# Kernel tuning notes

Hardware: AMD Instinct MI355X
Metric: run time of the kernel (lower is better)

The kernel has to match this reference:

```python
import jax, jax.numpy as jnp
import numpy as np

N = 100000
E = 1600000
IN_DIM, HID, OUT_DIM = 128, 128, 64


def setup_inputs() -> dict:
    key = jax.random.key(0)
    ks = jax.random.split(key, 8)
    x = jax.random.normal(ks[0], (N, IN_DIM), dtype=jnp.float32)
    edge_index = jax.random.randint(ks[1], (2, E), 0, N, dtype=jnp.int64)
    def glorot(k, fan_in, fan_out):
        lim = np.sqrt(6.0 / (fan_in + fan_out)).astype(np.float32)
        return jax.random.uniform(k, (fan_in, fan_out), jnp.float32, -lim, lim)
    W1 = glorot(ks[2], IN_DIM, HID)
    b1 = jnp.zeros((HID,), jnp.float32)
    W2 = glorot(ks[3], HID, HID)
    b2 = jnp.zeros((HID,), jnp.float32)
    W3 = glorot(ks[4], HID, OUT_DIM)
    b3 = jnp.zeros((OUT_DIM,), jnp.float32)
    return {"x": x, "edge_index": edge_index, "W1": W1, "b1": b1,
            "W2": W2, "b2": b2, "W3": W3, "b3": b3}


def _gcn_norm(edge_index, num_nodes):
    # PyG gcn_norm with add_self_loops=True, edge_weight=1:
    # A_hat = A + I, deg over destination (col), norm = d^-1/2[src]*d^-1/2[dst]
    loop = jnp.arange(num_nodes, dtype=edge_index.dtype)
    src = jnp.concatenate([edge_index[0], loop])
    dst = jnp.concatenate([edge_index[1], loop])
    deg = jax.ops.segment_sum(jnp.ones_like(dst, dtype=jnp.float32), dst,
                              num_segments=num_nodes)
    dinv = jnp.where(deg > 0, jax.lax.rsqrt(deg), 0.0)
    norm = dinv[src] * dinv[dst]  # [E + N]
    return src, dst, norm


def _gcn_conv(x, W, b, src, dst, norm, num_nodes):
    h = x @ W                                   # [N, out] linear transform
    msg = h[src] * norm[:, None]                # gather + normalize
    out = jax.ops.segment_sum(msg, dst, num_segments=num_nodes)  # scatter-add
    return out + b


def reference(x, edge_index, W1, b1, W2, b2, W3, b3):
    num_nodes = x.shape[0]
    src, dst, norm = _gcn_norm(edge_index, num_nodes)
    h = jax.nn.relu(_gcn_conv(x, W1, b1, src, dst, norm, num_nodes))
    h = jax.nn.relu(_gcn_conv(h, W2, b2, src, dst, norm, num_nodes))
    out = _gcn_conv(h, W3, b3, src, dst, norm, num_nodes)
    return out
```

## Files before the change

### kernel.cpp

```cpp
#include <hip/hip_runtime.h>
#include <hip/hip_bf16.h>

typedef __attribute__((ext_vector_type(8))) short bf16x8;
typedef __attribute__((ext_vector_type(4))) float f32x4;

#define NPB 32
#define BCAP 768
#define NSHARD 8
#define SCAP 160
#define CURSTRIDE 16


static __device__ __forceinline__ unsigned short f2bf(float f) {
    unsigned int u = __float_as_uint(f);
    unsigned int r = (u + 0x7fffu + ((u >> 16) & 1u)) >> 16;
    return (unsigned short)r;
}
static __device__ __forceinline__ float bflo(unsigned int v) {
    return __uint_as_float(v << 16);
}
static __device__ __forceinline__ float bfhi(unsigned int v) {
    return __uint_as_float(v & 0xffff0000u);
}


__global__ void k_bin(const int* __restrict__ src, const int* __restrict__ dst, int E,
                      int NB, int* __restrict__ scur, unsigned* __restrict__ recs) {
    int e = blockIdx.x * blockDim.x + threadIdx.x;
    const int shard = blockIdx.x & (NSHARD - 1);
    if (e < E) {
        int s = src[e], d = dst[e];
        int b = d >> 5;
        int pos = atomicAdd(&scur[(shard * NB + b) * CURSTRIDE], 1);
        if (pos < SCAP)
            recs[((size_t)shard * NB + b) * SCAP + pos] = ((unsigned)s << 5) | (unsigned)(d & 31);
    }
}

__global__ __launch_bounds__(256) void k_build(const unsigned* __restrict__ recs,
                                               const int* __restrict__ scur, int n, int NB,
                                               float* __restrict__ dinv,
                                               int* __restrict__ rp, int* __restrict__ re,
                                               int* __restrict__ col) {
    __shared__ unsigned lrec[BCAP];
    __shared__ int c32[NPB], x32[NPB], cur32[NPB];
    const int b = blockIdx.x;
    const int t = threadIdx.x;
    const size_t base = (size_t)b * BCAP;

    int cp[NSHARD + 1];
    cp[0] = 0;
#pragma unroll
    for (int s = 0; s < NSHARD; ++s) {
        int c = scur[(s * NB + b) * CURSTRIDE];
        c = (c < SCAP) ? c : SCAP;
        cp[s + 1] = cp[s] + c;
    }
    const int cnt = (cp[NSHARD] < BCAP) ? cp[NSHARD] : BCAP;

#pragma unroll
    for (int s = 0; s < NSHARD; ++s) {
        const unsigned* seg = recs + ((size_t)s * NB + b) * SCAP;
        const int c = cp[s + 1] - cp[s];
        for (int k = t; k < c; k += 256) {
            int o = cp[s] + k;
            if (o < BCAP) lrec[o] = seg[k];
        }
    }
    if (t < NPB) c32[t] = 0;
    __syncthreads();
    for (int k = t; k < cnt; k += 256) atomicAdd(&c32[lrec[k] & (NPB - 1)], 1);
    __syncthreads();
    if (t == 0) {
        int run = 0;
        for (int j = 0; j < NPB; ++j) { x32[j] = run; run += c32[j]; }
    }
    __syncthreads();
    if (t < NPB) {
        int node = b * NPB + t;
        if (node < n) {
            dinv[node] = rsqrtf((float)c32[t] + 1.0f);
            rp[node] = (int)base + x32[t];
            re[node] = (int)base + x32[t] + c32[t];
        }
        cur32[t] = x32[t];
    }
    __syncthreads();
    for (int k = t; k < cnt; k += 256) {
        unsigned r = lrec[k];
        int node = r & (NPB - 1);
        int slot = atomicAdd(&cur32[node], 1);
        col[base + slot] = (int)(r >> 5);
    }
}


__global__ void k_wsplit(const float* __restrict__ W, int C,
                         unsigned short* __restrict__ Wt_hi,
                         unsigned short* __restrict__ Wt_lo) {
    int idx = blockIdx.x * 256 + threadIdx.x;
    if (idx >= C * 128) return;
    int c = idx >> 7;
    int k = idx & 127;
    float a = W[k * C + c];
    unsigned short h = f2bf(a);
    float hf = __uint_as_float((unsigned int)h << 16);
    Wt_hi[idx] = h;
    Wt_lo[idx] = f2bf(a - hf);
}


template <int OUTD, bool BF16OUT>
__global__ __launch_bounds__(512, 4) void k_gemm_mfma(
    const float* __restrict__ A, const unsigned short* __restrict__ Wt_hi,
    const unsigned short* __restrict__ Wt_lo, void* __restrict__ houtp,
    int ntiles) {
    __shared__ unsigned short Ah[32 * 128];
    __shared__ unsigned short Al[32 * 128];
    const int t = threadIdx.x;
    const int wave = t >> 6, lane = t & 63;
    const int l15 = lane & 15, l4 = lane >> 4;

    const int cb = (OUTD == 128) ? wave : (wave & 3);
    const int s0 = (OUTD == 128) ? 0 : (wave >> 2);

    bf16x8 wh[4], wl[4];
    {
        const int c = cb * 16 + l15;
#pragma unroll
        for (int kk = 0; kk < 4; ++kk) {
            const int off = c * 128 + kk * 32 + l4 * 8;
            wh[kk] = *(const bf16x8*)&Wt_hi[off];
            wl[kk] = *(const bf16x8*)&Wt_lo[off];
        }
    }

    const int srow = t >> 4;
    const int sk0 = (t & 15) * 8;
    const int sboff = (srow * 256 + sk0 * 2) ^ ((srow & 7) << 4);

    for (int mt = blockIdx.x; mt < ntiles; mt += gridDim.x) {
        __syncthreads();
        {
            const float* src = A + ((size_t)mt * 32 + srow) * 128 + sk0;
            float4 a0 = *(const float4*)src;
            float4 a1 = *(const float4*)(src + 4);
            float av[8] = {a0.x, a0.y, a0.z, a0.w, a1.x, a1.y, a1.z, a1.w};
            bf16x8 hv, lv;
#pragma unroll
            for (int j = 0; j < 8; ++j) {
                unsigned short h = f2bf(av[j]);
                float hf = __uint_as_float((unsigned int)h << 16);
                hv[j] = (short)h;
                lv[j] = (short)f2bf(av[j] - hf);
            }
            *(bf16x8*)((char*)Ah + sboff) = hv;
            *(bf16x8*)((char*)Al + sboff) = lv;
        }
        __syncthreads();

        f32x4 acc0 = {0.f, 0.f, 0.f, 0.f};
        f32x4 acc1 = {0.f, 0.f, 0.f, 0.f};
        const int row0 = s0 * 16 + l15;
        const int xo = (l15 & 7) << 4;
#pragma unroll
        for (int kk = 0; kk < 4; ++kk) {
            const int off = kk * 64 + l4 * 16;
            bf16x8 a0h = *(const bf16x8*)((const char*)Ah + ((row0 * 256 + off) ^ xo));
            bf16x8 a0l = *(const bf16x8*)((const char*)Al + ((row0 * 256 + off) ^ xo));
            if (OUTD == 128) {
                bf16x8 a1h = *(const bf16x8*)((const char*)Ah + (((16 + l15) * 256 + off) ^ xo));
                bf16x8 a1l = *(const bf16x8*)((const char*)Al + (((16 + l15) * 256 + off) ^ xo));
                acc0 = __builtin_amdgcn_mfma_f32_16x16x32_bf16(a0h, wh[kk], acc0, 0, 0, 0);
                acc1 = __builtin_amdgcn_mfma_f32_16x16x32_bf16(a1h, wh[kk], acc1, 0, 0, 0);
                acc0 = __builtin_amdgcn_mfma_f32_16x16x32_bf16(a0l, wh[kk], acc0, 0, 0, 0);
                acc1 = __builtin_amdgcn_mfma_f32_16x16x32_bf16(a1l, wh[kk], acc1, 0, 0, 0);
                acc0 = __builtin_amdgcn_mfma_f32_16x16x32_bf16(a0h, wl[kk], acc0, 0, 0, 0);
                acc1 = __builtin_amdgcn_mfma_f32_16x16x32_bf16(a1h, wl[kk], acc1, 0, 0, 0);
            } else {
                acc0 = __builtin_amdgcn_mfma_f32_16x16x32_bf16(a0h, wh[kk], acc0, 0, 0, 0);
                acc0 = __builtin_amdgcn_mfma_f32_16x16x32_bf16(a0l, wh[kk], acc0, 0, 0, 0);
                acc0 = __builtin_amdgcn_mfma_f32_16x16x32_bf16(a0h, wl[kk], acc0, 0, 0, 0);
            }
        }

        const size_t rbase = (size_t)mt * 32;
        const int c = cb * 16 + l15;
#pragma unroll
        for (int q = 0; q < 4; ++q) {
            size_t r0 = rbase + (size_t)(s0 * 16 + l4 * 4 + q);
            if (BF16OUT) {
                ((unsigned short*)houtp)[r0 * OUTD + c] = f2bf(acc0[q]);
            } else {
                ((float*)houtp)[r0 * OUTD + c] = acc0[q];
            }
            if (OUTD == 128) {
                size_t r1 = rbase + (size_t)(16 + l4 * 4 + q);
                if (BF16OUT) {
                    ((unsigned short*)houtp)[r1 * OUTD + c] = f2bf(acc1[q]);
                } else {
                    ((float*)houtp)[r1 * OUTD + c] = acc1[q];
                }
            }
        }
    }
}


template <bool RELU>
__global__ void k_agg128_bf16(const unsigned int* __restrict__ hb,
                              const int* __restrict__ rp, const int* __restrict__ re,
                              const int* __restrict__ col, const float* __restrict__ dinv,
                              const float* __restrict__ b, float2* __restrict__ out, int n) {
    const int i = blockIdx.x;
    const int t = threadIdx.x;
    const float di = dinv[i];
    unsigned int self = hb[(size_t)i * 64 + t];
    float2 bb = ((const float2*)b)[t];
    float acc0 = bb.x + di * di * bflo(self);
    float acc1 = bb.y + di * di * bfhi(self);
    int e = rp[i];
    const int e1 = re[i];
    for (; e + 4 <= e1; e += 4) {
        int s0 = col[e], s1 = col[e + 1], s2 = col[e + 2], s3 = col[e + 3];
        float w0 = dinv[s0] * di, w1 = dinv[s1] * di;
        float w2 = dinv[s2] * di, w3 = dinv[s3] * di;
        unsigned int v0 = hb[(size_t)s0 * 64 + t];
        unsigned int v1 = hb[(size_t)s1 * 64 + t];
        unsigned int v2 = hb[(size_t)s2 * 64 + t];
        unsigned int v3 = hb[(size_t)s3 * 64 + t];
        acc0 += w0 * bflo(v0); acc1 += w0 * bfhi(v0);
        acc0 += w1 * bflo(v1); acc1 += w1 * bfhi(v1);
        acc0 += w2 * bflo(v2); acc1 += w2 * bfhi(v2);
        acc0 += w3 * bflo(v3); acc1 += w3 * bfhi(v3);
    }
    for (; e < e1; ++e) {
        int s = col[e];
        float w = dinv[s] * di;
        unsigned int v = hb[(size_t)s * 64 + t];
        acc0 += w * bflo(v); acc1 += w * bfhi(v);
    }
    if (RELU) { acc0 = fmaxf(acc0, 0.0f); acc1 = fmaxf(acc1, 0.0f); }
    out[(size_t)i * 64 + t] = make_float2(acc0, acc1);
}


__global__ void k_agg64_f32(const float* __restrict__ h, const int* __restrict__ rp,
                            const int* __restrict__ re, const int* __restrict__ col,
                            const float* __restrict__ dinv, const float* __restrict__ b,
                            float* __restrict__ out, int n) {
    const int i = blockIdx.x;
    const int d = threadIdx.x;
    const float di = dinv[i];
    float acc = b[d] + di * di * h[(size_t)i * 64 + d];
    int e = rp[i];
    const int e1 = re[i];
    for (; e + 4 <= e1; e += 4) {
        int s0 = col[e], s1 = col[e + 1], s2 = col[e + 2], s3 = col[e + 3];
        float w0 = dinv[s0] * di, w1 = dinv[s1] * di;
        float w2 = dinv[s2] * di, w3 = dinv[s3] * di;
        acc += w0 * h[(size_t)s0 * 64 + d];
        acc += w1 * h[(size_t)s1 * 64 + d];
        acc += w2 * h[(size_t)s2 * 64 + d];
        acc += w3 * h[(size_t)s3 * 64 + d];
    }
    for (; e < e1; ++e) {
        int s = col[e];
        acc += dinv[s] * di * h[(size_t)s * 64 + d];
    }
    out[(size_t)i * 64 + d] = acc;
}


extern "C" void kernel_launch(void* const* d_in, const int* in_sizes, int n_in,
                              void* d_out, int out_size, void* d_ws, size_t ws_size,
                              hipStream_t stream) {
    const float* x  = (const float*)d_in[0];
    const int*   ei = (const int*)d_in[1];
    const float* W1 = (const float*)d_in[2];
    const float* b1 = (const float*)d_in[3];
    const float* W2 = (const float*)d_in[4];
    const float* b2 = (const float*)d_in[5];
    const float* W3 = (const float*)d_in[6];
    const float* b3 = (const float*)d_in[7];
    float* out = (float*)d_out;

    const int n = in_sizes[0] / 128;
    const int E = in_sizes[1] / 2;
    const int* srcA = ei;
    const int* dstA = ei + E;
    const int NB = (n + NPB - 1) / NPB;

    char* ws = (char*)d_ws;
    size_t off = 0;
    auto alloc = [&](size_t bytes) -> void* {
        off = (off + 255) & ~(size_t)255;
        void* p = ws + off;
        off += bytes;
        return p;
    };

    void*  h    = alloc((size_t)n * 128 * 2);
    float* agg  = (float*)alloc((size_t)n * 128 * 4);
    unsigned* recs = (unsigned*)agg;
    float* dinv = (float*)alloc((size_t)n * 4);
    int*   rp   = (int*)alloc((size_t)n * 4);
    int*   re   = (int*)alloc((size_t)n * 4);
    int*   scur = (int*)alloc((size_t)NSHARD * NB * CURSTRIDE * 4);
    int*   col  = (int*)alloc((size_t)NB * BCAP * 4);
    unsigned short* W1h = (unsigned short*)alloc(128 * 128 * 2);
    unsigned short* W1l = (unsigned short*)alloc(128 * 128 * 2);
    unsigned short* W2h = (unsigned short*)alloc(128 * 128 * 2);
    unsigned short* W2l = (unsigned short*)alloc(128 * 128 * 2);
    unsigned short* W3h = (unsigned short*)alloc(64 * 128 * 2);
    unsigned short* W3l = (unsigned short*)alloc(64 * 128 * 2);

    hipMemsetAsync(scur, 0, (size_t)NSHARD * NB * CURSTRIDE * 4, stream);
    k_bin<<<(E + 255) / 256, 256, 0, stream>>>(srcA, dstA, E, NB, scur, recs);
    k_build<<<NB, 256, 0, stream>>>(recs, scur, n, NB, dinv, rp, re, col);

    k_wsplit<<<(128 * 128 + 255) / 256, 256, 0, stream>>>(W1, 128, W1h, W1l);
    k_wsplit<<<(128 * 128 + 255) / 256, 256, 0, stream>>>(W2, 128, W2h, W2l);
    k_wsplit<<<(64 * 128 + 255) / 256, 256, 0, stream>>>(W3, 64, W3h, W3l);

    const int ntiles = n / 32;
    const int gblocks = 1024;

    k_gemm_mfma<128, true><<<gblocks, 512, 0, stream>>>(x, W1h, W1l, h, ntiles);
    k_agg128_bf16<true><<<n, 64, 0, stream>>>((const unsigned int*)h, rp, re, col, dinv, b1,
                                              (float2*)agg, n);
    k_gemm_mfma<128, true><<<gblocks, 512, 0, stream>>>(agg, W2h, W2l, h, ntiles);
    k_agg128_bf16<true><<<n, 64, 0, stream>>>((const unsigned int*)h, rp, re, col, dinv, b2,
                                              (float2*)agg, n);
    k_gemm_mfma<64, false><<<gblocks, 512, 0, stream>>>(agg, W3h, W3l, h, ntiles);
    k_agg64_f32<<<n, 64, 0, stream>>>((const float*)h, rp, re, col, dinv, b3, out, n);
}
```

Measured before the change: 443.9 us.

## Store intermediate activations in bf16 and gather bf16 features in final aggregation

Aggregation outputs are now written as packed bf16 instead of fp32. The next GEMM loads them directly into shared memory and drops the low-part split and its MFMA pass. The last GEMM now emits bf16, and a new 64-wide aggregation kernel packs 8 nodes per 256-thread block and gathers bf16 pairs. The three weight-split launches are merged into one. This halves gather and intermediate traffic and removes some MFMA work, at the cost of extra rounding error on intermediate activations.

```diff
diff --git a/kernel.cpp b/kernel.cpp
--- a/kernel.cpp
+++ b/kernel.cpp
@@ -95,28 +95,36 @@
 }
 
 
-__global__ void k_wsplit(const float* __restrict__ W, int C,
-                         unsigned short* __restrict__ Wt_hi,
-                         unsigned short* __restrict__ Wt_lo) {
+__global__ void k_wsplit_all(const float* __restrict__ W1, const float* __restrict__ W2,
+                             const float* __restrict__ W3,
+                             unsigned short* __restrict__ W1h, unsigned short* __restrict__ W1l,
+                             unsigned short* __restrict__ W2h, unsigned short* __restrict__ W2l,
+                             unsigned short* __restrict__ W3h, unsigned short* __restrict__ W3l) {
     int idx = blockIdx.x * 256 + threadIdx.x;
-    if (idx >= C * 128) return;
+    const float* W;
+    unsigned short *Wh, *Wl;
+    int C;
+    if (idx < 16384) { W = W1; Wh = W1h; Wl = W1l; C = 128; }
+    else if (idx < 32768) { idx -= 16384; W = W2; Wh = W2h; Wl = W2l; C = 128; }
+    else if (idx < 40960) { idx -= 32768; W = W3; Wh = W3h; Wl = W3l; C = 64; }
+    else return;
     int c = idx >> 7;
     int k = idx & 127;
     float a = W[k * C + c];
     unsigned short h = f2bf(a);
     float hf = __uint_as_float((unsigned int)h << 16);
-    Wt_hi[idx] = h;
-    Wt_lo[idx] = f2bf(a - hf);
-}
-
-
-template <int OUTD, bool BF16OUT>
+    Wh[idx] = h;
+    Wl[idx] = f2bf(a - hf);
+}
+
+
+template <int OUTD, bool AF32, bool BF16OUT>
 __global__ __launch_bounds__(512, 4) void k_gemm_mfma(
-    const float* __restrict__ A, const unsigned short* __restrict__ Wt_hi,
+    const void* __restrict__ Ap, const unsigned short* __restrict__ Wt_hi,
     const unsigned short* __restrict__ Wt_lo, void* __restrict__ houtp,
     int ntiles) {
     __shared__ unsigned short Ah[32 * 128];
-    __shared__ unsigned short Al[32 * 128];
+    __shared__ unsigned short Al[AF32 ? 32 * 128 : 64];
     const int t = threadIdx.x;
     const int wave = t >> 6, lane = t & 63;
     const int l15 = lane & 15, l4 = lane >> 4;
@@ -141,8 +149,8 @@
 
     for (int mt = blockIdx.x; mt < ntiles; mt += gridDim.x) {
         __syncthreads();
-        {
-            const float* src = A + ((size_t)mt * 32 + srow) * 128 + sk0;
+        if (AF32) {
+            const float* src = (const float*)Ap + ((size_t)mt * 32 + srow) * 128 + sk0;
             float4 a0 = *(const float4*)src;
             float4 a1 = *(const float4*)(src + 4);
             float av[8] = {a0.x, a0.y, a0.z, a0.w, a1.x, a1.y, a1.z, a1.w};
@@ -156,6 +164,10 @@
             }
             *(bf16x8*)((char*)Ah + sboff) = hv;
             *(bf16x8*)((char*)Al + sboff) = lv;
+        } else {
+            const unsigned short* src =
+                (const unsigned short*)Ap + ((size_t)mt * 32 + srow) * 128 + sk0;
+            *(bf16x8*)((char*)Ah + sboff) = *(const bf16x8*)src;
         }
         __syncthreads();
 
@@ -167,20 +179,25 @@
         for (int kk = 0; kk < 4; ++kk) {
             const int off = kk * 64 + l4 * 16;
             bf16x8 a0h = *(const bf16x8*)((const char*)Ah + ((row0 * 256 + off) ^ xo));
-            bf16x8 a0l = *(const bf16x8*)((const char*)Al + ((row0 * 256 + off) ^ xo));
             if (OUTD == 128) {
                 bf16x8 a1h = *(const bf16x8*)((const char*)Ah + (((16 + l15) * 256 + off) ^ xo));
-                bf16x8 a1l = *(const bf16x8*)((const char*)Al + (((16 + l15) * 256 + off) ^ xo));
                 acc0 = __builtin_amdgcn_mfma_f32_16x16x32_bf16(a0h, wh[kk], acc0, 0, 0, 0);
                 acc1 = __builtin_amdgcn_mfma_f32_16x16x32_bf16(a1h, wh[kk], acc1, 0, 0, 0);
-                acc0 = __builtin_amdgcn_mfma_f32_16x16x32_bf16(a0l, wh[kk], acc0, 0, 0, 0);
-                acc1 = __builtin_amdgcn_mfma_f32_16x16x32_bf16(a1l, wh[kk], acc1, 0, 0, 0);
                 acc0 = __builtin_amdgcn_mfma_f32_16x16x32_bf16(a0h, wl[kk], acc0, 0, 0, 0);
                 acc1 = __builtin_amdgcn_mfma_f32_16x16x32_bf16(a1h, wl[kk], acc1, 0, 0, 0);
+                if (AF32) {
+                    bf16x8 a0l = *(const bf16x8*)((const char*)Al + ((row0 * 256 + off) ^ xo));
+                    bf16x8 a1l = *(const bf16x8*)((const char*)Al + (((16 + l15) * 256 + off) ^ xo));
+                    acc0 = __builtin_amdgcn_mfma_f32_16x16x32_bf16(a0l, wh[kk], acc0, 0, 0, 0);
+                    acc1 = __builtin_amdgcn_mfma_f32_16x16x32_bf16(a1l, wh[kk], acc1, 0, 0, 0);
+                }
             } else {
                 acc0 = __builtin_amdgcn_mfma_f32_16x16x32_bf16(a0h, wh[kk], acc0, 0, 0, 0);
-                acc0 = __builtin_amdgcn_mfma_f32_16x16x32_bf16(a0l, wh[kk], acc0, 0, 0, 0);
                 acc0 = __builtin_amdgcn_mfma_f32_16x16x32_bf16(a0h, wl[kk], acc0, 0, 0, 0);
+                if (AF32) {
+                    bf16x8 a0l = *(const bf16x8*)((const char*)Al + ((row0 * 256 + off) ^ xo));
+                    acc0 = __builtin_amdgcn_mfma_f32_16x16x32_bf16(a0l, wh[kk], acc0, 0, 0, 0);
+                }
             }
         }
 
@@ -211,7 +228,8 @@
 __global__ void k_agg128_bf16(const unsigned int* __restrict__ hb,
                               const int* __restrict__ rp, const int* __restrict__ re,
                               const int* __restrict__ col, const float* __restrict__ dinv,
-                              const float* __restrict__ b, float2* __restrict__ out, int n) {
+                              const float* __restrict__ b, unsigned int* __restrict__ outb,
+                              int n) {
     const int i = blockIdx.x;
     const int t = threadIdx.x;
     const float di = dinv[i];
@@ -241,34 +259,45 @@
         acc0 += w * bflo(v); acc1 += w * bfhi(v);
     }
     if (RELU) { acc0 = fmaxf(acc0, 0.0f); acc1 = fmaxf(acc1, 0.0f); }
-    out[(size_t)i * 64 + t] = make_float2(acc0, acc1);
-}
-
-
-__global__ void k_agg64_f32(const float* __restrict__ h, const int* __restrict__ rp,
-                            const int* __restrict__ re, const int* __restrict__ col,
-                            const float* __restrict__ dinv, const float* __restrict__ b,
-                            float* __restrict__ out, int n) {
-    const int i = blockIdx.x;
-    const int d = threadIdx.x;
+    outb[(size_t)i * 64 + t] = (unsigned)f2bf(acc0) | ((unsigned)f2bf(acc1) << 16);
+}
+
+
+__global__ void k_agg64_bf16(const unsigned int* __restrict__ hb,
+                             const int* __restrict__ rp, const int* __restrict__ re,
+                             const int* __restrict__ col, const float* __restrict__ dinv,
+                             const float* __restrict__ b, float2* __restrict__ out, int n) {
+    const int t = threadIdx.x;
+    const int i = blockIdx.x * 8 + (t >> 5);
+    const int ln = t & 31;
+    if (i >= n) return;
     const float di = dinv[i];
-    float acc = b[d] + di * di * h[(size_t)i * 64 + d];
+    unsigned int self = hb[(size_t)i * 32 + ln];
+    float2 bb = ((const float2*)b)[ln];
+    float acc0 = bb.x + di * di * bflo(self);
+    float acc1 = bb.y + di * di * bfhi(self);
     int e = rp[i];
     const int e1 = re[i];
     for (; e + 4 <= e1; e += 4) {
         int s0 = col[e], s1 = col[e + 1], s2 = col[e + 2], s3 = col[e + 3];
         float w0 = dinv[s0] * di, w1 = dinv[s1] * di;
         float w2 = dinv[s2] * di, w3 = dinv[s3] * di;
-        acc += w0 * h[(size_t)s0 * 64 + d];
-        acc += w1 * h[(size_t)s1 * 64 + d];
-        acc += w2 * h[(size_t)s2 * 64 + d];
-        acc += w3 * h[(size_t)s3 * 64 + d];
+        unsigned int v0 = hb[(size_t)s0 * 32 + ln];
+        unsigned int v1 = hb[(size_t)s1 * 32 + ln];
+        unsigned int v2 = hb[(size_t)s2 * 32 + ln];
+        unsigned int v3 = hb[(size_t)s3 * 32 + ln];
+        acc0 += w0 * bflo(v0); acc1 += w0 * bfhi(v0);
+        acc0 += w1 * bflo(v1); acc1 += w1 * bfhi(v1);
+        acc0 += w2 * bflo(v2); acc1 += w2 * bfhi(v2);
+        acc0 += w3 * bflo(v3); acc1 += w3 * bfhi(v3);
     }
     for (; e < e1; ++e) {
         int s = col[e];
-        acc += dinv[s] * di * h[(size_t)s * 64 + d];
-    }
-    out[(size_t)i * 64 + d] = acc;
+        float w = dinv[s] * di;
+        unsigned int v = hb[(size_t)s * 32 + ln];
+        acc0 += w * bflo(v); acc1 += w * bfhi(v);
+    }
+    out[(size_t)i * 32 + ln] = make_float2(acc0, acc1);
 }
 
 
@@ -301,7 +330,7 @@
     };
 
     void*  h    = alloc((size_t)n * 128 * 2);
-    float* agg  = (float*)alloc((size_t)n * 128 * 4);
+    void*  agg  = alloc((size_t)n * 128 * 2);
     unsigned* recs = (unsigned*)agg;
     float* dinv = (float*)alloc((size_t)n * 4);
     int*   rp   = (int*)alloc((size_t)n * 4);
@@ -319,19 +348,18 @@
     k_bin<<<(E + 255) / 256, 256, 0, stream>>>(srcA, dstA, E, NB, scur, recs);
     k_build<<<NB, 256, 0, stream>>>(recs, scur, n, NB, dinv, rp, re, col);
 
-    k_wsplit<<<(128 * 128 + 255) / 256, 256, 0, stream>>>(W1, 128, W1h, W1l);
-    k_wsplit<<<(128 * 128 + 255) / 256, 256, 0, stream>>>(W2, 128, W2h, W2l);
-    k_wsplit<<<(64 * 128 + 255) / 256, 256, 0, stream>>>(W3, 64, W3h, W3l);
+    k_wsplit_all<<<160, 256, 0, stream>>>(W1, W2, W3, W1h, W1l, W2h, W2l, W3h, W3l);
 
     const int ntiles = n / 32;
     const int gblocks = 1024;
 
-    k_gemm_mfma<128, true><<<gblocks, 512, 0, stream>>>(x, W1h, W1l, h, ntiles);
+    k_gemm_mfma<128, true, true><<<gblocks, 512, 0, stream>>>(x, W1h, W1l, h, ntiles);
     k_agg128_bf16<true><<<n, 64, 0, stream>>>((const unsigned int*)h, rp, re, col, dinv, b1,
-                                              (float2*)agg, n);
-    k_gemm_mfma<128, true><<<gblocks, 512, 0, stream>>>(agg, W2h, W2l, h, ntiles);
+                                              (unsigned int*)agg, n);
+    k_gemm_mfma<128, false, true><<<gblocks, 512, 0, stream>>>(agg, W2h, W2l, h, ntiles);
     k_agg128_bf16<true><<<n, 64, 0, stream>>>((const unsigned int*)h, rp, re, col, dinv, b2,
-                                              (float2*)agg, n);
-    k_gemm_mfma<64, false><<<gblocks, 512, 0, stream>>>(agg, W3h, W3l, h, ntiles);
-    k_agg64_f32<<<n, 64, 0, stream>>>((const float*)h, rp, re, col, dinv, b3, out, n);
-}
+                                              (unsigned int*)agg, n);
+    k_gemm_mfma<64, false, true><<<gblocks, 512, 0, stream>>>(agg, W3h, W3l, h, ntiles);
+    k_agg64_bf16<<<(n + 7) / 8, 256, 0, stream>>>((const unsigned int*)h, rp, re, col, dinv, b3,
+                                                  (float2*)out, n);
+}
```

Measured after the change: 405.6 us. -8.6%, faster.
